# Optimization experiments

Measured on AMD Instinct MI355X. Metric: run time of the kernel, lower is better.

## Reference

```python
import jax, jax.numpy as jnp
import numpy as np

H = 512

def _lstm_dir(seq, Wih, Whh, bih, bhh, reverse):
    # seq: [B,S,in]; Wih: [4H,in]; Whh: [4H,H]; biases [4H]
    B = seq.shape[0]
    xp = jnp.einsum('bsi,gi->bsg', seq, Wih) + bih  # precompute input projection [B,S,4H]
    h0 = jnp.zeros((B, H), seq.dtype)
    c0 = jnp.zeros((B, H), seq.dtype)

    def step(carry, xt):
        h, c = carry
        g = xt + h @ Whh.T + bhh
        i, f, gg, o = jnp.split(g, 4, axis=-1)
        c = jax.nn.sigmoid(f) * c + jax.nn.sigmoid(i) * jnp.tanh(gg)
        h = jax.nn.sigmoid(o) * jnp.tanh(c)
        return (h, c), h

    _, hs = jax.lax.scan(step, (h0, c0), jnp.swapaxes(xp, 0, 1), reverse=reverse)
    return jnp.swapaxes(hs, 0, 1)  # [B,S,H]


def setup_inputs() -> dict:
    key = jax.random.key(0)
    ks = jax.random.split(key, 24)
    B, S, E, V, C = 32, 512, 512, 32000, 2
    sc = 0.1
    d = {
        'x': jax.random.randint(ks[0], (B, S), 0, V, dtype=jnp.int32),
        'attention_mask': jnp.ones((B, S), dtype=jnp.int32),
        'emb': jax.random.normal(ks[1], (V, E), jnp.float32) * sc,
        'fc_W': jax.random.normal(ks[2], (C, 2 * H), jnp.float32) * sc,
        'fc_b': jax.random.normal(ks[3], (C,), jnp.float32) * sc,
    }
    i = 4
    for l, insz in [(0, E), (1, 2 * H)]:
        for dname in ('fwd', 'bwd'):
            d[f'{dname}_Wih{l}'] = jax.random.normal(ks[i], (4 * H, insz), jnp.float32) * sc; i += 1
            d[f'{dname}_Whh{l}'] = jax.random.normal(ks[i], (4 * H, H), jnp.float32) * sc; i += 1
            d[f'{dname}_bih{l}'] = jax.random.normal(ks[i], (4 * H,), jnp.float32) * sc; i += 1
            d[f'{dname}_bhh{l}'] = jax.random.normal(ks[i], (4 * H,), jnp.float32) * sc; i += 1
    return d


def reference(x, attention_mask, emb, fc_W, fc_b,
              fwd_Wih0, fwd_Whh0, fwd_bih0, fwd_bhh0,
              bwd_Wih0, bwd_Whh0, bwd_bih0, bwd_bhh0,
              fwd_Wih1, fwd_Whh1, fwd_bih1, fwd_bhh1,
              bwd_Wih1, bwd_Whh1, bwd_bih1, bwd_bhh1):
    out = emb[x]  # [B,S,E]
    layers = [
        ((fwd_Wih0, fwd_Whh0, fwd_bih0, fwd_bhh0), (bwd_Wih0, bwd_Whh0, bwd_bih0, bwd_bhh0)),
        ((fwd_Wih1, fwd_Whh1, fwd_bih1, fwd_bhh1), (bwd_Wih1, bwd_Whh1, bwd_bih1, bwd_bhh1)),
    ]
    for fw, bw in layers:
        f = _lstm_dir(out, *fw, reverse=False)
        b = _lstm_dir(out, *bw, reverse=True)
        out = jnp.concatenate([f, b], axis=-1)  # [B,S,2H]
        # dropout is identity in eval mode
    mask = attention_mask.astype(out.dtype)
    pooled = (out * mask[..., None]).sum(axis=1) / jnp.clip(mask.sum(axis=1, keepdims=True), 1e-9)
    logits = pooled @ fc_W.T + fc_b
    return logits
```

## Files before the change

### kernel.cpp

```cpp
#include <hip/hip_runtime.h>

typedef unsigned short u16;
typedef unsigned int   u32;
typedef unsigned long long u64;
typedef __attribute__((ext_vector_type(8))) short bf16x8;
typedef __attribute__((ext_vector_type(4))) float f32x4;

__device__ __forceinline__ u16 f2bf(float f) {
    u32 u; __builtin_memcpy(&u, &f, 4);
    u32 r = (u + 0x7FFFu + ((u >> 16) & 1u)) >> 16;
    return (u16)r;
}
__device__ __forceinline__ float bf2f(u16 h) {
    u32 u = ((u32)h) << 16; float f; __builtin_memcpy(&f, &u, 4); return f;
}
__device__ __forceinline__ float sigmoidf(float x) { return 1.f / (1.f + __expf(-x)); }
__device__ __forceinline__ float tanh_safe(float x) {
    float e = __expf(-2.f * fabsf(x));
    float t = (1.f - e) / (1.f + e);
    return x >= 0.f ? t : -t;
}

__global__ __launch_bounds__(256) void castk2(const float* __restrict__ s, u16* __restrict__ hi,
                                              u16* __restrict__ lo, int n) {
    int i = blockIdx.x * 256 + threadIdx.x;
    if (i < n) {
        float f = s[i];
        u16 h = f2bf(f);
        hi[i] = h;
        lo[i] = f2bf(f - bf2f(h));
    }
}

__global__ __launch_bounds__(256) void embed_cast(const int* __restrict__ x, const float* __restrict__ emb,
                                                  u16* __restrict__ x0) {
    int m = blockIdx.x;
    int idx = x[m];
    const float2* src = (const float2*)(emb + (size_t)idx * 512);
    u16* dst = x0 + (size_t)m * 512;
    int t = threadIdx.x;
    float2 v = src[t];
    dst[t * 2]     = f2bf(v.x);
    dst[t * 2 + 1] = f2bf(v.y);
}

__global__ __launch_bounds__(256) void gemm_bt(const u16* __restrict__ A, const u16* __restrict__ Bhi,
                                               const u16* __restrict__ Blo,
                                               u16* __restrict__ C, int M, int N, int K) {
    __shared__ __align__(16) u16 sA[128 * 32];
    __shared__ __align__(16) u16 sBh[128 * 32];
    __shared__ __align__(16) u16 sBl[128 * 32];
    const int tid  = threadIdx.x;
    const int lane = tid & 63, wave = tid >> 6;
    const int m0 = blockIdx.y * 128, n0 = blockIdx.x * 128;
    const int wm = (wave >> 1) * 64, wn = (wave & 1) * 64;
    f32x4 acc[4][4] = {};

    const int r0 = tid >> 2, c8 = (tid & 3) * 8;
    const int r1 = r0 + 64;
    const u16* Ap   = A   + (size_t)(m0 + r0) * K + c8;
    const u16* Ap2  = A   + (size_t)(m0 + r1) * K + c8;
    const u16* Bhp  = Bhi + (size_t)(n0 + r0) * K + c8;
    const u16* Bhp2 = Bhi + (size_t)(n0 + r1) * K + c8;
    const u16* Blp  = Blo + (size_t)(n0 + r0) * K + c8;
    const u16* Blp2 = Blo + (size_t)(n0 + r1) * K + c8;

    uint4 ra0, ra1, rh0, rh1, rl0, rl1;
    ra0 = *(const uint4*)(Ap);   ra1 = *(const uint4*)(Ap2);
    rh0 = *(const uint4*)(Bhp);  rh1 = *(const uint4*)(Bhp2);
    rl0 = *(const uint4*)(Blp);  rl1 = *(const uint4*)(Blp2);

    for (int kk = 0; kk < K; kk += 32) {
        __syncthreads();
        *(uint4*)(sA  + tid * 8)        = ra0;
        *(uint4*)(sA  + 2048 + tid * 8) = ra1;
        *(uint4*)(sBh + tid * 8)        = rh0;
        *(uint4*)(sBh + 2048 + tid * 8) = rh1;
        *(uint4*)(sBl + tid * 8)        = rl0;
        *(uint4*)(sBl + 2048 + tid * 8) = rl1;
        int kn = kk + 32;
        if (kn < K) {
            ra0 = *(const uint4*)(Ap + kn);   ra1 = *(const uint4*)(Ap2 + kn);
            rh0 = *(const uint4*)(Bhp + kn);  rh1 = *(const uint4*)(Bhp2 + kn);
            rl0 = *(const uint4*)(Blp + kn);  rl1 = *(const uint4*)(Blp2 + kn);
        }
        __syncthreads();
        bf16x8 av[4], bh[4], bl[4];
#pragma unroll
        for (int i = 0; i < 4; ++i) {
            av[i] = *(const bf16x8*)(sA  + (wm + i * 16 + (lane & 15)) * 32 + (lane >> 4) * 8);
            bh[i] = *(const bf16x8*)(sBh + (wn + i * 16 + (lane & 15)) * 32 + (lane >> 4) * 8);
            bl[i] = *(const bf16x8*)(sBl + (wn + i * 16 + (lane & 15)) * 32 + (lane >> 4) * 8);
        }
#pragma unroll
        for (int i = 0; i < 4; ++i)
#pragma unroll
            for (int j = 0; j < 4; ++j) {
                acc[i][j] = __builtin_amdgcn_mfma_f32_16x16x32_bf16(av[i], bh[j], acc[i][j], 0, 0, 0);
                acc[i][j] = __builtin_amdgcn_mfma_f32_16x16x32_bf16(av[i], bl[j], acc[i][j], 0, 0, 0);
            }
    }
#pragma unroll
    for (int i = 0; i < 4; ++i) {
        int m = m0 + wm + i * 16 + ((lane >> 4) << 2);
#pragma unroll
        for (int j = 0; j < 4; ++j) {
            int n = n0 + wn + j * 16 + (lane & 15);
#pragma unroll
            for (int rr = 0; rr < 4; ++rr)
                C[(size_t)(m + rr) * N + n] = f2bf(acc[i][j][rr]);
        }
    }
}

template <int LAYER>
__global__ __launch_bounds__(256, 1) void lstm_rec(
    const u16* __restrict__ xp_f, const u16* __restrict__ xp_b,
    const u16* __restrict__ whh_f_hi, const u16* __restrict__ whh_f_lo,
    const u16* __restrict__ whh_b_hi, const u16* __restrict__ whh_b_lo,
    const float* __restrict__ bih_f, const float* __restrict__ bhh_f,
    const float* __restrict__ bih_b, const float* __restrict__ bhh_b,
    u16* __restrict__ out0, float* __restrict__ pooled, const int* __restrict__ mask,
    u16* hbuf, u32* cnt)
{
    const int HP = 524;
    __shared__ __align__(16) u16  sHhi[32 * 524];
    __shared__ __align__(16) u16  sHlo[32 * 524];
    __shared__ __align__(16) float sG[32 * 33];

    const int tid = threadIdx.x;
    const int dir = blockIdx.x >> 6;
    const int slice = blockIdx.x & 63;
    const u16* xp     = dir ? xp_b : xp_f;
    const u16* whhH   = dir ? whh_b_hi : whh_f_hi;
    const u16* whhL   = dir ? whh_b_lo : whh_f_lo;
    const float* bih  = dir ? bih_b : bih_f;
    const float* bhh  = dir ? bhh_b : bhh_f;
    u16* hbD = hbuf + dir * 65536;
    u32* myFlags = cnt + dir * 256;

    const int wave = tid >> 6, lane = tid & 63;
    const int wm = (wave >> 1) * 16;
    const int wn = (wave & 1) * 16;
    bf16x8 wfragH[16], wfragL[16];
    {
        int n = wn + (lane & 15);
        int q = n >> 3, rr = n & 7;
        size_t rowoff = (size_t)(q * 512 + slice * 8 + rr) * 512 + (lane >> 4) * 8;
        const u16* wrh = whhH + rowoff;
        const u16* wrl = whhL + rowoff;
#pragma unroll
        for (int k2 = 0; k2 < 16; ++k2) {
            wfragH[k2] = *(const bf16x8*)(wrh + k2 * 32);
            wfragL[k2] = *(const bf16x8*)(wrl + k2 * 32);
        }
    }
    const int b = tid >> 3, r = tid & 7;
    float bias[4];
#pragma unroll
    for (int q = 0; q < 4; ++q) {
        int g = q * 512 + slice * 8 + r;
        bias[q] = bih[g] + bhh[g];
    }
    float cstate = 0.f, pool = 0.f;
    const int aoff = (wm + (lane & 15)) * HP + (lane >> 4) * 8;
    const int gRow = wm + ((lane >> 4) << 2), gCol = wn + (lane & 15);
    const int srow = tid >> 3, sc = tid & 7;
    const u16* xpBase = xp + (size_t)(b * 512) * 2048 + slice * 8 + r;

    for (int t = 0; t < 512; ++t) {
        const int tt = dir ? (511 - t) : t;
        const u16* xrow = xpBase + (size_t)tt * 2048;
        u16 xv0 = xrow[0], xv1 = xrow[512], xv2 = xrow[1024], xv3 = xrow[1536];
        if (t > 0 && tid < 64) {
            const u32 tgt = (u32)t;
            const u64* fp = (const u64*)(myFlags + tid * 4);
            for (;;) {
                u64 f01 = __hip_atomic_load(fp,     __ATOMIC_RELAXED, __HIP_MEMORY_SCOPE_AGENT);
                u64 f23 = __hip_atomic_load(fp + 1, __ATOMIC_RELAXED, __HIP_MEMORY_SCOPE_AGENT);
                int ok = ((u32)f01 >= tgt) & ((u32)(f01 >> 32) >= tgt) &
                         ((u32)f23 >= tgt) & ((u32)(f23 >> 32) >= tgt);
                if (__all(ok)) break;
                __builtin_amdgcn_s_sleep(1);
            }
            __builtin_amdgcn_fence(__ATOMIC_ACQUIRE, "agent");
        }
        __syncthreads();
        if (t > 0) {
            const uint4* hp4 = (const uint4*)(hbD + ((t - 1) & 1) * 32768 + srow * 512);
            const uint4* lp4 = (const uint4*)(hbD + ((t - 1) & 1) * 32768 + 16384 + srow * 512);
            u16* dhi = sHhi + srow * HP;
            u16* dlo = sHlo + srow * HP;
            uint4 rh[8], rl[8];
#pragma unroll
            for (int j = 0; j < 8; ++j) {
                int ch = sc + 8 * j;
                rh[j] = hp4[ch];
                rl[j] = lp4[ch];
            }
#pragma unroll
            for (int j = 0; j < 8; ++j) {
                int ch = sc + 8 * j;
                *(uint4*)(dhi + ch * 8) = rh[j];
                *(uint4*)(dlo + ch * 8) = rl[j];
            }
        }
        __syncthreads();
        f32x4 ac0 = {}, ac1 = {}, ac2 = {};
        if (t > 0) {
#pragma unroll
            for (int k2 = 0; k2 < 16; ++k2) {
                bf16x8 ah = *(const bf16x8*)(sHhi + aoff + k2 * 32);
                bf16x8 al = *(const bf16x8*)(sHlo + aoff + k2 * 32);
                ac0 = __builtin_amdgcn_mfma_f32_16x16x32_bf16(ah, wfragH[k2], ac0, 0, 0, 0);
                ac1 = __builtin_amdgcn_mfma_f32_16x16x32_bf16(al, wfragH[k2], ac1, 0, 0, 0);
                ac2 = __builtin_amdgcn_mfma_f32_16x16x32_bf16(ah, wfragL[k2], ac2, 0, 0, 0);
            }
        }
#pragma unroll
        for (int rr = 0; rr < 4; ++rr) sG[(gRow + rr) * 33 + gCol] = ac0[rr] + ac1[rr] + ac2[rr];
        __syncthreads();
        {
            float gq[4];
            gq[0] = sG[b * 33 + 0 * 8 + r] + bf2f(xv0) + bias[0];
            gq[1] = sG[b * 33 + 1 * 8 + r] + bf2f(xv1) + bias[1];
            gq[2] = sG[b * 33 + 2 * 8 + r] + bf2f(xv2) + bias[2];
            gq[3] = sG[b * 33 + 3 * 8 + r] + bf2f(xv3) + bias[3];
            float ig = sigmoidf(gq[0]), fg = sigmoidf(gq[1]);
            float gg = tanh_safe(gq[2]), og = sigmoidf(gq[3]);
            cstate = fg * cstate + ig * gg;
            float h = og * tanh_safe(cstate);
            u16 hh = f2bf(h);
            u16 hl = f2bf(h - bf2f(hh));
            if (LAYER == 0) {
                out0[((size_t)(b * 512 + tt)) * 1024 + dir * 512 + slice * 8 + r] = hh;
            } else {
                pool += h * (float)mask[b * 512 + tt];
            }
            u16* gh = hbD + (t & 1) * 32768 + b * 512 + slice * 8 + r;
            __hip_atomic_store(gh,         hh, __ATOMIC_RELAXED, __HIP_MEMORY_SCOPE_AGENT);
            __hip_atomic_store(gh + 16384, hl, __ATOMIC_RELAXED, __HIP_MEMORY_SCOPE_AGENT);
            asm volatile("s_waitcnt vmcnt(0)" ::: "memory");
            if (lane == 0)
                __hip_atomic_store(myFlags + slice * 4 + wave, (u32)(t + 1),
                                   __ATOMIC_RELAXED, __HIP_MEMORY_SCOPE_AGENT);
        }
    }
    if (LAYER == 1)
        pooled[(size_t)b * 1024 + dir * 512 + slice * 8 + r] = pool;
}

__global__ __launch_bounds__(256) void final_fc(const float* __restrict__ pooled, const int* __restrict__ mask,
                                                const float* __restrict__ fcW, const float* __restrict__ fcb,
                                                float* __restrict__ out) {
    __shared__ float red[256];
    int tid = threadIdx.x;
    int pair = tid & 63, kc = tid >> 6;
    int b = pair >> 1, c = pair & 1;
    float s = 0.f;
    for (int k = kc * 256; k < kc * 256 + 256; ++k)
        s += pooled[b * 1024 + k] * fcW[c * 1024 + k];
    red[tid] = s;
    __syncthreads();
    if (kc == 0) {
        float tot = red[pair] + red[64 + pair] + red[128 + pair] + red[192 + pair];
        float ms = 0.f;
        for (int t = 0; t < 512; ++t) ms += (float)mask[b * 512 + t];
        ms = fmaxf(ms, 1e-9f);
        out[b * 2 + c] = tot / ms + fcb[c];
    }
}

extern "C" void kernel_launch(void* const* d_in, const int* in_sizes, int n_in,
                              void* d_out, int out_size, void* d_ws, size_t ws_size,
                              hipStream_t stream) {
    (void)in_sizes; (void)n_in; (void)out_size; (void)ws_size;
    const int*   x     = (const int*)d_in[0];
    const int*   amask = (const int*)d_in[1];
    const float* emb   = (const float*)d_in[2];
    const float* fcW   = (const float*)d_in[3];
    const float* fcb   = (const float*)d_in[4];
    const float* fWih0 = (const float*)d_in[5];
    const float* fWhh0 = (const float*)d_in[6];
    const float* fbih0 = (const float*)d_in[7];
    const float* fbhh0 = (const float*)d_in[8];
    const float* bWih0 = (const float*)d_in[9];
    const float* bWhh0 = (const float*)d_in[10];
    const float* bbih0 = (const float*)d_in[11];
    const float* bbhh0 = (const float*)d_in[12];
    const float* fWih1 = (const float*)d_in[13];
    const float* fWhh1 = (const float*)d_in[14];
    const float* fbih1 = (const float*)d_in[15];
    const float* fbhh1 = (const float*)d_in[16];
    const float* bWih1 = (const float*)d_in[17];
    const float* bWhh1 = (const float*)d_in[18];
    const float* bbih1 = (const float*)d_in[19];
    const float* bbhh1 = (const float*)d_in[20];

    char* ws = (char*)d_ws;
    size_t off = 0;
    auto alloc = [&](size_t bytes) { void* p = ws + off; off += (bytes + 1023) & ~(size_t)1023; return p; };
    u16* x0    = (u16*)alloc((size_t)16384 * 512 * 2);
    u16* xpf   = (u16*)alloc((size_t)16384 * 2048 * 2);
    u16* xpb   = (u16*)alloc((size_t)16384 * 2048 * 2);
    u16* out0  = (u16*)alloc((size_t)16384 * 1024 * 2);
    u16* wih0fH = (u16*)alloc((size_t)2048 * 512 * 2);
    u16* wih0fL = (u16*)alloc((size_t)2048 * 512 * 2);
    u16* wih0bH = (u16*)alloc((size_t)2048 * 512 * 2);
    u16* wih0bL = (u16*)alloc((size_t)2048 * 512 * 2);
    u16* whh0fH = (u16*)alloc((size_t)2048 * 512 * 2);
    u16* whh0fL = (u16*)alloc((size_t)2048 * 512 * 2);
    u16* whh0bH = (u16*)alloc((size_t)2048 * 512 * 2);
    u16* whh0bL = (u16*)alloc((size_t)2048 * 512 * 2);
    u16* wih1fH = (u16*)alloc((size_t)2048 * 1024 * 2);
    u16* wih1fL = (u16*)alloc((size_t)2048 * 1024 * 2);
    u16* wih1bH = (u16*)alloc((size_t)2048 * 1024 * 2);
    u16* wih1bL = (u16*)alloc((size_t)2048 * 1024 * 2);
    u16* whh1fH = (u16*)alloc((size_t)2048 * 512 * 2);
    u16* whh1fL = (u16*)alloc((size_t)2048 * 512 * 2);
    u16* whh1bH = (u16*)alloc((size_t)2048 * 512 * 2);
    u16* whh1bL = (u16*)alloc((size_t)2048 * 512 * 2);
    float* pooled = (float*)alloc((size_t)32 * 1024 * 4);
    u16* hbuf  = (u16*)alloc((size_t)2 * 2 * 2 * 32 * 512 * 2);
    u32* cnt   = (u32*)alloc(4096);

    hipMemsetAsync(cnt, 0, 4096, stream);

    const int NW0 = 2048 * 512, NW1 = 2048 * 1024;
    castk2<<<dim3((NW0 + 255) / 256), 256, 0, stream>>>(fWih0, wih0fH, wih0fL, NW0);
    castk2<<<dim3((NW0 + 255) / 256), 256, 0, stream>>>(bWih0, wih0bH, wih0bL, NW0);
    castk2<<<dim3((NW0 + 255) / 256), 256, 0, stream>>>(fWhh0, whh0fH, whh0fL, NW0);
    castk2<<<dim3((NW0 + 255) / 256), 256, 0, stream>>>(bWhh0, whh0bH, whh0bL, NW0);
    castk2<<<dim3((NW1 + 255) / 256), 256, 0, stream>>>(fWih1, wih1fH, wih1fL, NW1);
    castk2<<<dim3((NW1 + 255) / 256), 256, 0, stream>>>(bWih1, wih1bH, wih1bL, NW1);
    castk2<<<dim3((NW0 + 255) / 256), 256, 0, stream>>>(fWhh1, whh1fH, whh1fL, NW0);
    castk2<<<dim3((NW0 + 255) / 256), 256, 0, stream>>>(bWhh1, whh1bH, whh1bL, NW0);

    embed_cast<<<dim3(16384), 256, 0, stream>>>(x, emb, x0);

    gemm_bt<<<dim3(16, 128), 256, 0, stream>>>(x0, wih0fH, wih0fL, xpf, 16384, 2048, 512);
    gemm_bt<<<dim3(16, 128), 256, 0, stream>>>(x0, wih0bH, wih0bL, xpb, 16384, 2048, 512);
    lstm_rec<0><<<dim3(128), 256, 0, stream>>>(xpf, xpb, whh0fH, whh0fL, whh0bH, whh0bL,
                                               fbih0, fbhh0, bbih0, bbhh0,
                                               out0, nullptr, nullptr, hbuf, cnt);
    gemm_bt<<<dim3(16, 128), 256, 0, stream>>>(out0, wih1fH, wih1fL, xpf, 16384, 2048, 1024);
    gemm_bt<<<dim3(16, 128), 256, 0, stream>>>(out0, wih1bH, wih1bL, xpb, 16384, 2048, 1024);
    lstm_rec<1><<<dim3(128), 256, 0, stream>>>(xpf, xpb, whh1fH, whh1fL, whh1bH, whh1bL,
                                               fbih1, fbhh1, bbih1, bbhh1,
                                               nullptr, pooled, amask, hbuf, cnt + 512);

    final_fc<<<dim3(1), 256, 0, stream>>>(pooled, amask, fcW, fcb, (float*)d_out);
}
```

Before: 6.624 ms.

## Pack h values with step tags into 64-bit words to drop flag synchronization

Replaces the per-wave flag counters and acquire fence with self-validating 64-bit words that hold hi/lo bf16 h plus a step tag. Each thread polls its own slice of h directly and re-reads only stale entries, which removes the store-wait, flag store, flag polling round trip and one __syncthreads per step. Shared memory now holds packed hi/lo pairs that are unpacked before the MFMAs, so each step does more global traffic (8 bytes per element) and extra ALU work for unpacking. It also needs 64 u64 registers per thread, which raises register pressure.

```diff
diff --git a/kernel.cpp b/kernel.cpp
--- a/kernel.cpp
+++ b/kernel.cpp
@@ -121,11 +121,9 @@
     const float* __restrict__ bih_f, const float* __restrict__ bhh_f,
     const float* __restrict__ bih_b, const float* __restrict__ bhh_b,
     u16* __restrict__ out0, float* __restrict__ pooled, const int* __restrict__ mask,
-    u16* hbuf, u32* cnt)
+    u64* hbuf)
 {
-    const int HP = 524;
-    __shared__ __align__(16) u16  sHhi[32 * 524];
-    __shared__ __align__(16) u16  sHlo[32 * 524];
+    __shared__ __align__(16) u32  sH[32 * 516];
     __shared__ __align__(16) float sG[32 * 33];
 
     const int tid = threadIdx.x;
@@ -136,17 +134,17 @@
     const u16* whhL   = dir ? whh_b_lo : whh_f_lo;
     const float* bih  = dir ? bih_b : bih_f;
     const float* bhh  = dir ? bhh_b : bhh_f;
-    u16* hbD = hbuf + dir * 65536;
-    u32* myFlags = cnt + dir * 256;
+    u64* hbD = hbuf + dir * 32768;
 
     const int wave = tid >> 6, lane = tid & 63;
+    const int l15 = lane & 15, lk8 = (lane >> 4) * 8;
     const int wm = (wave >> 1) * 16;
     const int wn = (wave & 1) * 16;
     bf16x8 wfragH[16], wfragL[16];
     {
-        int n = wn + (lane & 15);
+        int n = wn + l15;
         int q = n >> 3, rr = n & 7;
-        size_t rowoff = (size_t)(q * 512 + slice * 8 + rr) * 512 + (lane >> 4) * 8;
+        size_t rowoff = (size_t)(q * 512 + slice * 8 + rr) * 512 + lk8;
         const u16* wrh = whhH + rowoff;
         const u16* wrl = whhL + rowoff;
 #pragma unroll
@@ -163,58 +161,68 @@
         bias[q] = bih[g] + bhh[g];
     }
     float cstate = 0.f, pool = 0.f;
-    const int aoff = (wm + (lane & 15)) * HP + (lane >> 4) * 8;
+    const int aoff = (wm + l15) * 516 + lk8;
     const int gRow = wm + ((lane >> 4) << 2), gCol = wn + (lane & 15);
     const int srow = tid >> 3, sc = tid & 7;
     const u16* xpBase = xp + (size_t)(b * 512) * 2048 + slice * 8 + r;
 
     for (int t = 0; t < 512; ++t) {
         const int tt = dir ? (511 - t) : t;
+        const u32 tgt = (u32)(LAYER * 512 + t);
+        const u64* src = hbD + (size_t)((t - 1) & 1) * 16384 + srow * 512;
+        u64 v[64];
+        if (t > 0) {
+#pragma unroll
+            for (int j = 0; j < 8; ++j)
+#pragma unroll
+                for (int m = 0; m < 8; ++m)
+                    v[j * 8 + m] = __hip_atomic_load(src + j * 64 + m * 8 + sc,
+                                                     __ATOMIC_RELAXED, __HIP_MEMORY_SCOPE_AGENT);
+        }
         const u16* xrow = xpBase + (size_t)tt * 2048;
         u16 xv0 = xrow[0], xv1 = xrow[512], xv2 = xrow[1024], xv3 = xrow[1536];
-        if (t > 0 && tid < 64) {
-            const u32 tgt = (u32)t;
-            const u64* fp = (const u64*)(myFlags + tid * 4);
+        int mv = (LAYER == 1) ? mask[b * 512 + tt] : 0;
+        if (t > 0) {
             for (;;) {
-                u64 f01 = __hip_atomic_load(fp,     __ATOMIC_RELAXED, __HIP_MEMORY_SCOPE_AGENT);
-                u64 f23 = __hip_atomic_load(fp + 1, __ATOMIC_RELAXED, __HIP_MEMORY_SCOPE_AGENT);
-                int ok = ((u32)f01 >= tgt) & ((u32)(f01 >> 32) >= tgt) &
-                         ((u32)f23 >= tgt) & ((u32)(f23 >> 32) >= tgt);
-                if (__all(ok)) break;
-                __builtin_amdgcn_s_sleep(1);
+                u32 bad = 0;
+#pragma unroll
+                for (int e = 0; e < 64; ++e) bad |= (u32)v[e] ^ tgt;
+                if (__all(bad == 0)) break;
+#pragma unroll
+                for (int j = 0; j < 8; ++j)
+#pragma unroll
+                    for (int m = 0; m < 8; ++m)
+                        if ((u32)v[j * 8 + m] != tgt)
+                            v[j * 8 + m] = __hip_atomic_load(src + j * 64 + m * 8 + sc,
+                                                             __ATOMIC_RELAXED, __HIP_MEMORY_SCOPE_AGENT);
             }
-            __builtin_amdgcn_fence(__ATOMIC_ACQUIRE, "agent");
-        }
-        __syncthreads();
-        if (t > 0) {
-            const uint4* hp4 = (const uint4*)(hbD + ((t - 1) & 1) * 32768 + srow * 512);
-            const uint4* lp4 = (const uint4*)(hbD + ((t - 1) & 1) * 32768 + 16384 + srow * 512);
-            u16* dhi = sHhi + srow * HP;
-            u16* dlo = sHlo + srow * HP;
-            uint4 rh[8], rl[8];
-#pragma unroll
-            for (int j = 0; j < 8; ++j) {
-                int ch = sc + 8 * j;
-                rh[j] = hp4[ch];
-                rl[j] = lp4[ch];
-            }
-#pragma unroll
-            for (int j = 0; j < 8; ++j) {
-                int ch = sc + 8 * j;
-                *(uint4*)(dhi + ch * 8) = rh[j];
-                *(uint4*)(dlo + ch * 8) = rl[j];
-            }
+            u32* dst = sH + srow * 516;
+#pragma unroll
+            for (int j = 0; j < 8; ++j)
+#pragma unroll
+                for (int m = 0; m < 8; ++m)
+                    dst[j * 64 + m * 8 + sc] = (u32)(v[j * 8 + m] >> 32);
         }
         __syncthreads();
         f32x4 ac0 = {}, ac1 = {}, ac2 = {};
         if (t > 0) {
 #pragma unroll
             for (int k2 = 0; k2 < 16; ++k2) {
-                bf16x8 ah = *(const bf16x8*)(sHhi + aoff + k2 * 32);
-                bf16x8 al = *(const bf16x8*)(sHlo + aoff + k2 * 32);
-                ac0 = __builtin_amdgcn_mfma_f32_16x16x32_bf16(ah, wfragH[k2], ac0, 0, 0, 0);
-                ac1 = __builtin_amdgcn_mfma_f32_16x16x32_bf16(al, wfragH[k2], ac1, 0, 0, 0);
-                ac2 = __builtin_amdgcn_mfma_f32_16x16x32_bf16(ah, wfragL[k2], ac2, 0, 0, 0);
+                const u32* ap = sH + aoff + k2 * 32;
+                uint4 q0 = *(const uint4*)ap;
+                uint4 q1 = *(const uint4*)(ap + 4);
+                union { u32 w[4]; bf16x8 v8; } AH, AL;
+                AH.w[0] = (q0.x >> 16) | (q0.y & 0xFFFF0000u);
+                AL.w[0] = (q0.x & 0xFFFFu) | (q0.y << 16);
+                AH.w[1] = (q0.z >> 16) | (q0.w & 0xFFFF0000u);
+                AL.w[1] = (q0.z & 0xFFFFu) | (q0.w << 16);
+                AH.w[2] = (q1.x >> 16) | (q1.y & 0xFFFF0000u);
+                AL.w[2] = (q1.x & 0xFFFFu) | (q1.y << 16);
+                AH.w[3] = (q1.z >> 16) | (q1.w & 0xFFFF0000u);
+                AL.w[3] = (q1.z & 0xFFFFu) | (q1.w << 16);
+                ac0 = __builtin_amdgcn_mfma_f32_16x16x32_bf16(AH.v8, wfragH[k2], ac0, 0, 0, 0);
+                ac1 = __builtin_amdgcn_mfma_f32_16x16x32_bf16(AL.v8, wfragH[k2], ac1, 0, 0, 0);
+                ac2 = __builtin_amdgcn_mfma_f32_16x16x32_bf16(AH.v8, wfragL[k2], ac2, 0, 0, 0);
             }
         }
 #pragma unroll
@@ -232,18 +240,14 @@
             float h = og * tanh_safe(cstate);
             u16 hh = f2bf(h);
             u16 hl = f2bf(h - bf2f(hh));
+            u64 pv = ((u64)hh << 48) | ((u64)hl << 32) | (u64)(u32)(LAYER * 512 + t + 1);
+            __hip_atomic_store(hbD + (size_t)(t & 1) * 16384 + b * 512 + slice * 8 + r, pv,
+                               __ATOMIC_RELAXED, __HIP_MEMORY_SCOPE_AGENT);
             if (LAYER == 0) {
                 out0[((size_t)(b * 512 + tt)) * 1024 + dir * 512 + slice * 8 + r] = hh;
             } else {
-                pool += h * (float)mask[b * 512 + tt];
+                pool += h * (float)mv;
             }
-            u16* gh = hbD + (t & 1) * 32768 + b * 512 + slice * 8 + r;
-            __hip_atomic_store(gh,         hh, __ATOMIC_RELAXED, __HIP_MEMORY_SCOPE_AGENT);
-            __hip_atomic_store(gh + 16384, hl, __ATOMIC_RELAXED, __HIP_MEMORY_SCOPE_AGENT);
-            asm volatile("s_waitcnt vmcnt(0)" ::: "memory");
-            if (lane == 0)
-                __hip_atomic_store(myFlags + slice * 4 + wave, (u32)(t + 1),
-                                   __ATOMIC_RELAXED, __HIP_MEMORY_SCOPE_AGENT);
         }
     }
     if (LAYER == 1)
@@ -321,10 +325,9 @@
     u16* whh1bH = (u16*)alloc((size_t)2048 * 512 * 2);
     u16* whh1bL = (u16*)alloc((size_t)2048 * 512 * 2);
     float* pooled = (float*)alloc((size_t)32 * 1024 * 4);
-    u16* hbuf  = (u16*)alloc((size_t)2 * 2 * 2 * 32 * 512 * 2);
-    u32* cnt   = (u32*)alloc(4096);
-
-    hipMemsetAsync(cnt, 0, 4096, stream);
+    u64* hbuf  = (u64*)alloc((size_t)65536 * 8);
+
+    hipMemsetAsync(hbuf, 0, (size_t)65536 * 8, stream);
 
     const int NW0 = 2048 * 512, NW1 = 2048 * 1024;
     castk2<<<dim3((NW0 + 255) / 256), 256, 0, stream>>>(fWih0, wih0fH, wih0fL, NW0);
@@ -342,12 +345,12 @@
     gemm_bt<<<dim3(16, 128), 256, 0, stream>>>(x0, wih0bH, wih0bL, xpb, 16384, 2048, 512);
     lstm_rec<0><<<dim3(128), 256, 0, stream>>>(xpf, xpb, whh0fH, whh0fL, whh0bH, whh0bL,
                                                fbih0, fbhh0, bbih0, bbhh0,
-                                               out0, nullptr, nullptr, hbuf, cnt);
+                                               out0, nullptr, nullptr, hbuf);
     gemm_bt<<<dim3(16, 128), 256, 0, stream>>>(out0, wih1fH, wih1fL, xpf, 16384, 2048, 1024);
     gemm_bt<<<dim3(16, 128), 256, 0, stream>>>(out0, wih1bH, wih1bL, xpb, 16384, 2048, 1024);
     lstm_rec<1><<<dim3(128), 256, 0, stream>>>(xpf, xpb, whh1fH, whh1fL, whh1bH, whh1bL,
                                                fbih1, fbhh1, bbih1, bbhh1,
-                                               nullptr, pooled, amask, hbuf, cnt + 512);
+                                               nullptr, pooled, amask, hbuf);
 
     final_fc<<<dim3(1), 256, 0, stream>>>(pooled, amask, fcW, fcb, (float*)d_out);
 }
```

New measurement: 9.130 ms. +37.8%, slower.
